# Optimization experiments

Measured on AMD Instinct MI355X. Metric: run time of the kernel, lower is better.

Reference implementation:

```python
import jax, jax.numpy as jnp
import numpy as np

# ---- static config (from xib add_argument defaults / chosen production sizes) ----
B, L = 16, 50            # batch, text length
LU, KU, DIM = 60, 100, 60
V, MAXVL = 2000, 10      # vocab size, max vocab word length (J)
MIN_WL, MAX_WL = 4, 10   # min/max extracted word length
NE = MAX_WL - MIN_WL + 1 # number of len_e candidates
INS_DEL_COST = 3.5       # min_ins_del_cost
UNEXTRACTED_PROB = 0.01
CONTEXT_WEIGHT = 0.1     # weight for context (conv) log-probs
NEG = -9999.9


def setup_inputs() -> dict:
    key = jax.random.key(0)
    ks = jax.random.split(key, 8)
    unit_id_seqs = jax.random.randint(ks[0], (B, L), 0, LU)
    lengths = 10 + jax.random.randint(ks[1], (B,), 0, L - 9)  # in [10, L]
    unit_repr = jax.random.normal(ks[2], (KU, DIM), jnp.float32)
    aligner_weight = 0.1 * jax.random.normal(ks[3], (LU, KU), jnp.float32)
    conv_w = jax.random.normal(ks[4], (DIM, DIM, 3), jnp.float32) / np.sqrt(3.0 * DIM)
    conv_b = jnp.zeros((DIM,), jnp.float32)
    vocab_ids = jax.random.randint(ks[5], (V, MAXVL), 0, KU)
    vocab_lengths = MIN_WL + jax.random.randint(ks[6], (V,), 0, MAXVL - MIN_WL + 1)
    return dict(unit_id_seqs=unit_id_seqs, lengths=lengths, unit_repr=unit_repr,
                aligner_weight=aligner_weight, conv_w=conv_w, conv_b=conv_b,
                vocab_ids=vocab_ids, vocab_lengths=vocab_lengths)


def reference(unit_id_seqs, lengths, unit_repr, aligner_weight, conv_w, conv_b,
              vocab_ids, vocab_lengths):
    # ---- G2P layer: embedding-as-matmul + Conv1d over length ----
    ku_char_repr = aligner_weight @ unit_repr                 # (LU, DIM)
    emb = ku_char_repr[unit_id_seqs]                          # (B, L, DIM)
    x = jnp.swapaxes(emb, 1, 2)                               # (B, DIM, L)
    y = jax.lax.conv_general_dilated(x, conv_w, (1,), 'SAME',
                                     dimension_numbers=('NCH', 'OIH', 'NCH'))
    word_repr = jnp.swapaxes(y + conv_b[None, :, None], 1, 2)  # (B, L, DIM)
    char_log_probs = jax.nn.log_softmax(ku_char_repr @ unit_repr.T, axis=-1)  # (LU, KU)
    alignment = jnp.exp(char_log_probs)
    ctx_log_probs = jax.nn.log_softmax(word_repr @ unit_repr.T, axis=-1)      # (B, L, KU)
    # per-position substitution log prob against each known unit
    pos_lp = char_log_probs[unit_id_seqs] + CONTEXT_WEIGHT * ctx_log_probs    # (B, L, KU)
    sub = pos_lp[:, :, vocab_ids]                                             # (B, L, V, J)
    sub = jnp.pad(sub, ((0, 0), (0, MAX_WL), (0, 0), (0, 0)), constant_values=NEG)
    J = MAXVL
    # ---- edit-distance style DP over (span char i, vocab char j), vectorized
    # over (batch, start position, vocab). prev[b,s,j,v] = f[i-1][j].
    j_ar = jnp.arange(J + 1, dtype=sub.dtype)
    prev = jnp.broadcast_to((-INS_DEL_COST * j_ar)[None, None, :, None], (B, L, J + 1, V))
    vl_idx = jnp.broadcast_to(vocab_lengths[None, None, None, :].astype(jnp.int32), (B, L, 1, V))
    lls = []
    for i in range(1, MAX_WL + 1):          # fixed small loop (<=10)
        sub_i = sub[:, i - 1:i - 1 + L]     # (B, L, V, J): char at position s+i-1
        row = [jnp.full((B, L, V), -INS_DEL_COST * i, dtype=sub.dtype)]
        for j in range(1, J + 1):           # fixed small loop (<=10)
            diag = prev[:, :, j - 1, :] + sub_i[:, :, :, j - 1]
            up = prev[:, :, j, :] - INS_DEL_COST
            left = row[j - 1] - INS_DEL_COST
            row.append(jnp.maximum(diag, jnp.maximum(up, left)))
        prev = jnp.stack(row, axis=2)       # (B, L, J+1, V)
        if i >= MIN_WL:                     # matched ll for word length i
            lls.append(jnp.take_along_axis(prev, vl_idx, axis=2)[:, :, 0, :])
    ll = jnp.stack(lls, axis=2)             # (B, L, NE, V) = matches.ll
    # ---- viability mask + unextracted penalty, pick best candidate ----
    starts = jnp.arange(L)
    word_lens = MIN_WL + jnp.arange(NE)
    viable = (starts[None, :, None] + word_lens[None, None, :]) <= lengths[:, None, None]  # (B,L,NE)
    unextracted = (lengths[:, None, None] - word_lens[None, None, :]).astype(ll.dtype)     # (B,1,NE)
    score = (ll + jnp.where(viable, 0.0, NEG)[..., None]
             + (unextracted * np.log(UNEXTRACTED_PROB))[..., None, :, None][:, 0])
    flat = score.reshape(B, L * NE * V)
    best_idx = jnp.argmax(flat, axis=1)
    best_matched_ll = jnp.max(flat, axis=1)
    start = best_idx // (NE * V)
    e_idx = (best_idx // V) % NE
    best_matched_vocab = best_idx % V
    end = start + MIN_WL + e_idx - 1
    return start, end, best_matched_ll, best_matched_vocab, alignment
```

## Files before the change

kernel.cpp:

```cpp
#include <hip/hip_runtime.h>
#include <math.h>
#include <stdint.h>

#define B_ 16
#define L_ 50
#define LU_ 60
#define KU_ 100
#define DIM_ 60
#define V_ 2000
#define MAXVL_ 10
#define MIN_WL_ 4
#define MAX_WL_ 10
#define NE_ 7
#define IDC_ 3.5f
#define LOG_UNEXT_ (-4.6051701859880913680359829093687f)
#define CTXW_ 0.1f

#define WS_PLP  0
#define WS_BEST_BYTES (80000u * 4u)
#define BEST_STRIDE 8

#define URP_ 61
#define CWP_ 61
#define TSP_ 12

__global__ __launch_bounds__(256) void ctx_kernel(
    const int* __restrict__ uid,
    const float* __restrict__ unit_repr,
    const float* __restrict__ aligner_w,
    const float* __restrict__ conv_w,
    const float* __restrict__ conv_b,
    float* __restrict__ ws_plp,
    float* __restrict__ out_align,
    unsigned long long* __restrict__ g_best)
{
  int bl = blockIdx.x;
  int b = bl / L_, l = bl % L_;
  int t = threadIdx.x;
  __shared__ float s_ur[KU_ * URP_];
  __shared__ float s_cw[3 * DIM_ * CWP_];
  __shared__ float s_aw[3 * KU_];
  __shared__ float sx[3 * DIM_];
  __shared__ float s_kur[DIM_];
  __shared__ float swr[DIM_];
  __shared__ float sclp[KU_];
  __shared__ float slog[KU_];
  __shared__ float salg[KU_];
  __shared__ float sls[3];

  if (bl == 0 && t < B_) g_best[t * BEST_STRIDE] = 0ull;

  const float4* ur4 = (const float4*)unit_repr;
  for (int k = t; k < (KU_ * DIM_) / 4; k += 256) {
    float4 v = ur4[k];
    int i0 = 4 * k;
    s_ur[((i0 + 0) / DIM_) * URP_ + ((i0 + 0) % DIM_)] = v.x;
    s_ur[((i0 + 1) / DIM_) * URP_ + ((i0 + 1) % DIM_)] = v.y;
    s_ur[((i0 + 2) / DIM_) * URP_ + ((i0 + 2) % DIM_)] = v.z;
    s_ur[((i0 + 3) / DIM_) * URP_ + ((i0 + 3) % DIM_)] = v.w;
  }
  const float4* cw4 = (const float4*)conv_w;
  for (int k = t; k < (DIM_ * DIM_ * 3) / 4; k += 256) {
    float4 v = cw4[k];
    int i0 = 4 * k;
    float vv[4] = {v.x, v.y, v.z, v.w};
#pragma unroll
    for (int e = 0; e < 4; ++e) {
      int idx = i0 + e;
      int o = idx / (3 * DIM_), id = idx % (3 * DIM_);
      s_cw[id * CWP_ + o] = vv[e];
    }
  }
  int ud[3];
#pragma unroll
  for (int d = 0; d < 3; ++d) {
    int ld = l + d - 1;
    ud[d] = (ld >= 0 && ld < L_) ? uid[b * L_ + ld] : -1;
  }
  for (int i = t; i < 3 * KU_; i += 256) {
    int d = i / KU_, k = i - d * KU_;
    s_aw[i] = (ud[d] >= 0) ? aligner_w[ud[d] * KU_ + k] : 0.f;
  }
  __syncthreads();

  if (t < 3 * DIM_) {
    int d = t / DIM_, c = t - d * DIM_;
    float acc = 0.f;
    for (int k = 0; k < KU_; ++k) acc += s_aw[d * KU_ + k] * s_ur[k * URP_ + c];
    sx[t] = acc;
  } else if (bl < LU_ && t >= 192 && t < 192 + DIM_) {
    int c = t - 192;
    float acc = 0.f;
    for (int k = 0; k < KU_; ++k) acc += aligner_w[bl * KU_ + k] * s_ur[k * URP_ + c];
    s_kur[c] = acc;
  }
  __syncthreads();

  if (t < DIM_) {
    float acc = conv_b[t];
    for (int i = 0; i < DIM_; ++i) {
      acc += sx[0 * DIM_ + i] * s_cw[(i * 3 + 0) * CWP_ + t];
      acc += sx[1 * DIM_ + i] * s_cw[(i * 3 + 1) * CWP_ + t];
      acc += sx[2 * DIM_ + i] * s_cw[(i * 3 + 2) * CWP_ + t];
    }
    swr[t] = acc;
  } else if (t >= 64 && t < 64 + KU_) {
    int j = t - 64;
    float acc = 0.f;
    for (int d = 0; d < DIM_; ++d) acc += sx[DIM_ + d] * s_ur[j * URP_ + d];
    sclp[j] = acc;
  }
  __syncthreads();

  if (t < KU_) {
    float acc = 0.f;
    for (int d = 0; d < DIM_; ++d) acc += swr[d] * s_ur[t * URP_ + d];
    slog[t] = acc;
  } else if (bl < LU_ && t >= 128 && t < 128 + KU_) {
    int j = t - 128;
    float acc = 0.f;
    for (int d = 0; d < DIM_; ++d) acc += s_kur[d] * s_ur[j * URP_ + d];
    salg[j] = acc;
  }
  __syncthreads();

  {
    int w = t >> 6, lane = t & 63;
    int nred = (bl < LU_) ? 3 : 2;
    if (w < nred) {
      const float* arr = (w == 0) ? sclp : (w == 1) ? slog : salg;
      float v1 = arr[lane];
      float v2 = (lane < KU_ - 64) ? arr[64 + lane] : -1e30f;
      float mx = fmaxf(v1, v2);
#pragma unroll
      for (int off = 32; off > 0; off >>= 1)
        mx = fmaxf(mx, __shfl_xor(mx, off));
      float s = expf(v1 - mx) + ((lane < KU_ - 64) ? expf(v2 - mx) : 0.f);
#pragma unroll
      for (int off = 32; off > 0; off >>= 1)
        s += __shfl_xor(s, off);
      if (lane == 0) sls[w] = mx + logf(s);
    }
  }
  __syncthreads();

  if (t < KU_) {
    float pos = (sclp[t] - sls[0]) + CTXW_ * (slog[t] - sls[1]);
    ws_plp[bl * KU_ + t] = pos;
    if (bl < LU_) out_align[bl * KU_ + t] = expf(salg[t] - sls[2]);
  }
}

__global__ __launch_bounds__(256) void dp_kernel(
    const int* __restrict__ lengths,
    const int* __restrict__ vocab_ids,
    const int* __restrict__ vocab_lengths,
    const float* __restrict__ ws_plp,
    unsigned long long* __restrict__ g_best)
{
  int bl = blockIdx.x;
  int b = bl / L_, l = bl % L_;
  int len_b = lengths[b];
  int imax = len_b - l;
  if (imax > MAX_WL_) imax = MAX_WL_;
  if (imax < MIN_WL_) return;

  __shared__ float sT[KU_ * TSP_];
  __shared__ unsigned long long swave[4];
  int t = threadIdx.x;
  {
    int n = imax * KU_;
    for (int idx = t; idx < n; idx += 256) {
      int i = idx / KU_, k = idx - i * KU_;
      sT[k * TSP_ + i] = ws_plp[(bl + i) * KU_ + k];
    }
  }
  __syncthreads();

  int v0 = blockIdx.y * 512 + t;
  int v1 = v0 + 256;
  bool has1 = (v1 < V_);
  int vid0[MAXVL_], vid1[MAXVL_];
#pragma unroll
  for (int j = 0; j < MAXVL_; ++j) vid0[j] = vocab_ids[v0 * MAXVL_ + j];
  if (has1) {
#pragma unroll
    for (int j = 0; j < MAXVL_; ++j) vid1[j] = vocab_ids[v1 * MAXVL_ + j];
  } else {
#pragma unroll
    for (int j = 0; j < MAXVL_; ++j) vid1[j] = 0;
  }
  int vlen0 = vocab_lengths[v0];
  int vlen1 = has1 ? vocab_lengths[v1] : MIN_WL_;
  bool tail = (imax > 8);

  float A0[MAXVL_ + 1], A1[MAXVL_ + 1];
  float sv0[NE_], sv1[NE_];
#pragma unroll
  for (int e = 0; e < NE_; ++e) { sv0[e] = 0.f; sv1[e] = 0.f; }
#pragma unroll
  for (int i = 0; i <= MAXVL_; ++i) {
    A0[i] = -IDC_ * (float)i;
    A1[i] = A0[i];
  }

#pragma unroll
  for (int j = 1; j <= MAXVL_; ++j) {
    const float* c0 = &sT[vid0[j - 1] * TSP_];
    const float* c1 = &sT[vid1[j - 1] * TSP_];
    float4 a0 = *(const float4*)(c0);
    float4 m0 = *(const float4*)(c0 + 4);
    float4 a1 = *(const float4*)(c1);
    float4 m1 = *(const float4*)(c1 + 4);
    float2 e0 = make_float2(0.f, 0.f), e1 = make_float2(0.f, 0.f);
    if (tail) {
      e0 = *(const float2*)(c0 + 8);
      e1 = *(const float2*)(c1 + 8);
    }
    float s0[MAXVL_] = {a0.x, a0.y, a0.z, a0.w, m0.x, m0.y, m0.z, m0.w, e0.x, e0.y};
    float s1[MAXVL_] = {a1.x, a1.y, a1.z, a1.w, m1.x, m1.y, m1.z, m1.w, e1.x, e1.y};
    float B0[MAXVL_ + 1], B1[MAXVL_ + 1];
    B0[0] = -IDC_ * (float)j;
    B1[0] = B0[0];
#pragma unroll
    for (int i = 1; i <= MAXVL_; ++i) {
      B0[i] = fmaxf(A0[i - 1] + s0[i - 1], fmaxf(A0[i], B0[i - 1]) - IDC_);
      B1[i] = fmaxf(A1[i - 1] + s1[i - 1], fmaxf(A1[i], B1[i - 1]) - IDC_);
    }
    if (j == vlen0) {
#pragma unroll
      for (int e = 0; e < NE_; ++e) sv0[e] = B0[MIN_WL_ + e];
    }
    if (j == vlen1) {
#pragma unroll
      for (int e = 0; e < NE_; ++e) sv1[e] = B1[MIN_WL_ + e];
    }
#pragma unroll
    for (int i = 0; i <= MAXVL_; ++i) { A0[i] = B0[i]; A1[i] = B1[i]; }
  }

  unsigned long long bestKey = 0ull;
#pragma unroll
  for (int e = 0; e < NE_; ++e) {
    int i = MIN_WL_ + e;
    if (i <= imax) {
      float unext = (float)(len_b - i) * LOG_UNEXT_;
      unsigned int idx_base = (unsigned int)(l * (NE_ * V_) + e * V_);
      {
        float score = sv0[e] + unext;
        unsigned int u = __float_as_uint(score);
        u = (u & 0x80000000u) ? ~u : (u | 0x80000000u);
        unsigned long long key =
            ((unsigned long long)u << 32) |
            (unsigned long long)(~(idx_base + (unsigned int)v0));
        if (key > bestKey) bestKey = key;
      }
      if (has1) {
        float score = sv1[e] + unext;
        unsigned int u = __float_as_uint(score);
        u = (u & 0x80000000u) ? ~u : (u | 0x80000000u);
        unsigned long long key =
            ((unsigned long long)u << 32) |
            (unsigned long long)(~(idx_base + (unsigned int)v1));
        if (key > bestKey) bestKey = key;
      }
    }
  }

#pragma unroll
  for (int off = 32; off > 0; off >>= 1) {
    unsigned long long o = __shfl_down(bestKey, off);
    if (o > bestKey) bestKey = o;
  }
  int wid = t >> 6;
  if ((t & 63) == 0) swave[wid] = bestKey;
  __syncthreads();
  if (t == 0) {
    unsigned long long k0 = swave[0];
    for (int w = 1; w < 4; ++w)
      if (swave[w] > k0) k0 = swave[w];
    atomicMax(g_best + (size_t)b * BEST_STRIDE, k0);
  }
}

__global__ void decode_kernel(const unsigned long long* __restrict__ g_best,
                              float* __restrict__ out)
{
  int t = threadIdx.x;
  if (t < B_) {
    unsigned long long key = g_best[t * BEST_STRIDE];
    unsigned int u = (unsigned int)(key >> 32);
    unsigned int idx = ~((unsigned int)(key & 0xFFFFFFFFull));
    unsigned int bits = (u & 0x80000000u) ? (u & 0x7FFFFFFFu) : ~u;
    float val = __uint_as_float(bits);
    int start = (int)(idx / (NE_ * V_));
    int rem = (int)(idx % (NE_ * V_));
    int e = rem / V_;
    int vv = rem % V_;
    out[t] = (float)start;
    out[B_ + t] = (float)(start + MIN_WL_ + e - 1);
    out[2 * B_ + t] = val;
    out[3 * B_ + t] = (float)vv;
  }
}

extern "C" void kernel_launch(void* const* d_in, const int* in_sizes, int n_in,
                              void* d_out, int out_size, void* d_ws, size_t ws_size,
                              hipStream_t stream)
{
  const int* uid            = (const int*)d_in[0];
  const int* lengths        = (const int*)d_in[1];
  const float* unit_repr    = (const float*)d_in[2];
  const float* aligner_w    = (const float*)d_in[3];
  const float* conv_w       = (const float*)d_in[4];
  const float* conv_b       = (const float*)d_in[5];
  const int* vocab_ids      = (const int*)d_in[6];
  const int* vocab_lengths  = (const int*)d_in[7];
  float* out = (float*)d_out;
  float* ws_f = (float*)d_ws;
  unsigned long long* g_best =
      (unsigned long long*)((char*)d_ws + WS_BEST_BYTES);

  ctx_kernel<<<B_ * L_, 256, 0, stream>>>(uid, unit_repr, aligner_w, conv_w,
                                          conv_b, ws_f + WS_PLP, out + 4 * B_,
                                          g_best);
  dim3 g3(B_ * L_, 4);
  dp_kernel<<<g3, 256, 0, stream>>>(lengths, vocab_ids, vocab_lengths,
                                    ws_f + WS_PLP, g_best);
  decode_kernel<<<1, 64, 0, stream>>>(g_best, out);
}
```

Before: 118.1 us.

## Batch four text positions per ctx block and pack vocab ids in DP

The context kernel now handles four consecutive text positions per block (13 blocks per batch row instead of 50), so the unit_repr and conv weight staging into shared memory is amortised over more work and the embeddings of neighbouring positions are shared. The DP kernel packs the 10 vocab ids into three 32-bit registers as bytes to cut register pressure. It also folds the best-key computation into the DP loop at the matching word length, dropping the saved-value arrays. The tail-load guard is removed, so the DP always reads 10 columns from shared memory. Fewer ctx blocks means less parallelism in that stage.

```diff
diff --git a/kernel.cpp b/kernel.cpp
--- a/kernel.cpp
+++ b/kernel.cpp
@@ -15,6 +15,7 @@
 #define IDC_ 3.5f
 #define LOG_UNEXT_ (-4.6051701859880913680359829093687f)
 #define CTXW_ 0.1f
+#define NQ_ 13
 
 #define WS_PLP  0
 #define WS_BEST_BYTES (80000u * 4u)
@@ -34,21 +35,24 @@
     float* __restrict__ out_align,
     unsigned long long* __restrict__ g_best)
 {
-  int bl = blockIdx.x;
-  int b = bl / L_, l = bl % L_;
+  int blk = blockIdx.x;
+  int b = blk / NQ_, q = blk % NQ_;
+  int l0 = 4 * q;
+  int npos = (l0 + 4 <= L_) ? 4 : (L_ - l0);
+  int alr = (blk < LU_) ? blk : -1;
   int t = threadIdx.x;
+
   __shared__ float s_ur[KU_ * URP_];
   __shared__ float s_cw[3 * DIM_ * CWP_];
-  __shared__ float s_aw[3 * KU_];
-  __shared__ float sx[3 * DIM_];
-  __shared__ float s_kur[DIM_];
-  __shared__ float swr[DIM_];
-  __shared__ float sclp[KU_];
-  __shared__ float slog[KU_];
+  __shared__ float s_aw[7 * KU_];
+  __shared__ float s_kx[7 * DIM_];
+  __shared__ float swr[4 * DIM_];
+  __shared__ float sclp[4 * KU_];
+  __shared__ float sctx[4 * KU_];
   __shared__ float salg[KU_];
-  __shared__ float sls[3];
-
-  if (bl == 0 && t < B_) g_best[t * BEST_STRIDE] = 0ull;
+  __shared__ float sls[9];
+
+  if (blk == 0 && t < B_) g_best[t * BEST_STRIDE] = 0ull;
 
   const float4* ur4 = (const float4*)unit_repr;
   for (int k = t; k < (KU_ * DIM_) / 4; k += 256) {
@@ -71,84 +75,101 @@
       s_cw[id * CWP_ + o] = vv[e];
     }
   }
-  int ud[3];
-#pragma unroll
-  for (int d = 0; d < 3; ++d) {
-    int ld = l + d - 1;
-    ud[d] = (ld >= 0 && ld < L_) ? uid[b * L_ + ld] : -1;
-  }
-  for (int i = t; i < 3 * KU_; i += 256) {
-    int d = i / KU_, k = i - d * KU_;
-    s_aw[i] = (ud[d] >= 0) ? aligner_w[ud[d] * KU_ + k] : 0.f;
-  }
-  __syncthreads();
-
-  if (t < 3 * DIM_) {
-    int d = t / DIM_, c = t - d * DIM_;
+  for (int i = t; i < 7 * KU_; i += 256) {
+    int m = i / KU_, k = i - m * KU_;
+    float w = 0.f;
+    if (m < 6) {
+      int ld = l0 - 1 + m;
+      if (ld >= 0 && ld < L_) {
+        int u = uid[b * L_ + ld];
+        w = aligner_w[u * KU_ + k];
+      }
+    } else if (alr >= 0) {
+      w = aligner_w[alr * KU_ + k];
+    }
+    s_aw[i] = w;
+  }
+  __syncthreads();
+
+  for (int idx = t; idx < 7 * DIM_; idx += 256) {
+    int m = idx / DIM_, c = idx - m * DIM_;
     float acc = 0.f;
-    for (int k = 0; k < KU_; ++k) acc += s_aw[d * KU_ + k] * s_ur[k * URP_ + c];
-    sx[t] = acc;
-  } else if (bl < LU_ && t >= 192 && t < 192 + DIM_) {
-    int c = t - 192;
-    float acc = 0.f;
-    for (int k = 0; k < KU_; ++k) acc += aligner_w[bl * KU_ + k] * s_ur[k * URP_ + c];
-    s_kur[c] = acc;
-  }
-  __syncthreads();
-
-  if (t < DIM_) {
-    float acc = conv_b[t];
-    for (int i = 0; i < DIM_; ++i) {
-      acc += sx[0 * DIM_ + i] * s_cw[(i * 3 + 0) * CWP_ + t];
-      acc += sx[1 * DIM_ + i] * s_cw[(i * 3 + 1) * CWP_ + t];
-      acc += sx[2 * DIM_ + i] * s_cw[(i * 3 + 2) * CWP_ + t];
-    }
-    swr[t] = acc;
-  } else if (t >= 64 && t < 64 + KU_) {
-    int j = t - 64;
-    float acc = 0.f;
-    for (int d = 0; d < DIM_; ++d) acc += sx[DIM_ + d] * s_ur[j * URP_ + d];
-    sclp[j] = acc;
-  }
-  __syncthreads();
-
-  if (t < KU_) {
-    float acc = 0.f;
-    for (int d = 0; d < DIM_; ++d) acc += swr[d] * s_ur[t * URP_ + d];
-    slog[t] = acc;
-  } else if (bl < LU_ && t >= 128 && t < 128 + KU_) {
-    int j = t - 128;
-    float acc = 0.f;
-    for (int d = 0; d < DIM_; ++d) acc += s_kur[d] * s_ur[j * URP_ + d];
-    salg[j] = acc;
+    for (int k = 0; k < KU_; ++k) acc += s_aw[m * KU_ + k] * s_ur[k * URP_ + c];
+    s_kx[idx] = acc;
+  }
+  __syncthreads();
+
+  for (int idx = t; idx < 240 + 4 * KU_; idx += 256) {
+    if (idx < 240) {
+      int p = idx / DIM_, o = idx - p * DIM_;
+      float acc = conv_b[o];
+      for (int i = 0; i < DIM_; ++i) {
+        acc += s_kx[(p + 0) * DIM_ + i] * s_cw[(i * 3 + 0) * CWP_ + o];
+        acc += s_kx[(p + 1) * DIM_ + i] * s_cw[(i * 3 + 1) * CWP_ + o];
+        acc += s_kx[(p + 2) * DIM_ + i] * s_cw[(i * 3 + 2) * CWP_ + o];
+      }
+      swr[p * DIM_ + o] = acc;
+    } else {
+      int r = idx - 240;
+      int p = r / KU_, j = r - p * KU_;
+      float acc = 0.f;
+      for (int d = 0; d < DIM_; ++d) acc += s_kx[(p + 1) * DIM_ + d] * s_ur[j * URP_ + d];
+      sclp[r] = acc;
+    }
+  }
+  __syncthreads();
+
+  for (int idx = t; idx < 4 * KU_ + KU_; idx += 256) {
+    if (idx < 4 * KU_) {
+      int p = idx / KU_, j = idx - p * KU_;
+      float acc = 0.f;
+      for (int d = 0; d < DIM_; ++d) acc += swr[p * DIM_ + d] * s_ur[j * URP_ + d];
+      sctx[idx] = acc;
+    } else {
+      int j = idx - 4 * KU_;
+      float acc = 0.f;
+      for (int d = 0; d < DIM_; ++d) acc += s_kx[6 * DIM_ + d] * s_ur[j * URP_ + d];
+      salg[j] = acc;
+    }
   }
   __syncthreads();
 
   {
-    int w = t >> 6, lane = t & 63;
-    int nred = (bl < LU_) ? 3 : 2;
-    if (w < nred) {
-      const float* arr = (w == 0) ? sclp : (w == 1) ? slog : salg;
-      float v1 = arr[lane];
-      float v2 = (lane < KU_ - 64) ? arr[64 + lane] : -1e30f;
-      float mx = fmaxf(v1, v2);
-#pragma unroll
-      for (int off = 32; off > 0; off >>= 1)
-        mx = fmaxf(mx, __shfl_xor(mx, off));
-      float s = expf(v1 - mx) + ((lane < KU_ - 64) ? expf(v2 - mx) : 0.f);
-#pragma unroll
-      for (int off = 32; off > 0; off >>= 1)
-        s += __shfl_xor(s, off);
-      if (lane == 0) sls[w] = mx + logf(s);
-    }
-  }
-  __syncthreads();
-
-  if (t < KU_) {
-    float pos = (sclp[t] - sls[0]) + CTXW_ * (slog[t] - sls[1]);
-    ws_plp[bl * KU_ + t] = pos;
-    if (bl < LU_) out_align[bl * KU_ + t] = expf(salg[t] - sls[2]);
-  }
+    int g = t >> 5, lane = t & 31;
+#pragma unroll
+    for (int round = 0; round < 2; ++round) {
+      int r = round * 8 + g;
+      if (r < 9) {
+        const float* arr = (r == 8) ? salg
+                          : ((r & 1) ? &sctx[(r >> 1) * KU_] : &sclp[(r >> 1) * KU_]);
+        float v1 = arr[lane];
+        float v2 = arr[32 + lane];
+        float v3 = arr[64 + lane];
+        float v4 = (lane < KU_ - 96) ? arr[96 + lane] : -1e30f;
+        float mx = fmaxf(fmaxf(v1, v2), fmaxf(v3, v4));
+#pragma unroll
+        for (int off = 16; off > 0; off >>= 1)
+          mx = fmaxf(mx, __shfl_xor(mx, off));
+        float s = expf(v1 - mx) + expf(v2 - mx) + expf(v3 - mx) +
+                  ((lane < KU_ - 96) ? expf(v4 - mx) : 0.f);
+#pragma unroll
+        for (int off = 16; off > 0; off >>= 1)
+          s += __shfl_xor(s, off);
+        if (lane == 0) sls[r] = mx + logf(s);
+      }
+    }
+  }
+  __syncthreads();
+
+  for (int idx = t; idx < 4 * KU_; idx += 256) {
+    int p = idx / KU_, j = idx - p * KU_;
+    if (p < npos) {
+      float pos = (sclp[idx] - sls[2 * p]) + CTXW_ * (sctx[idx] - sls[2 * p + 1]);
+      ws_plp[(b * L_ + l0 + p) * KU_ + j] = pos;
+    }
+  }
+  if (alr >= 0 && t < KU_)
+    out_align[alr * KU_ + t] = expf(salg[t] - sls[8]);
 }
 
 __global__ __launch_bounds__(256) void dp_kernel(
@@ -180,43 +201,38 @@
   int v0 = blockIdx.y * 512 + t;
   int v1 = v0 + 256;
   bool has1 = (v1 < V_);
-  int vid0[MAXVL_], vid1[MAXVL_];
-#pragma unroll
-  for (int j = 0; j < MAXVL_; ++j) vid0[j] = vocab_ids[v0 * MAXVL_ + j];
+  unsigned p0[3] = {0u, 0u, 0u}, p1[3] = {0u, 0u, 0u};
+#pragma unroll
+  for (int j = 0; j < MAXVL_; ++j)
+    p0[j >> 2] |= ((unsigned)vocab_ids[v0 * MAXVL_ + j]) << ((j & 3) * 8);
   if (has1) {
 #pragma unroll
-    for (int j = 0; j < MAXVL_; ++j) vid1[j] = vocab_ids[v1 * MAXVL_ + j];
-  } else {
-#pragma unroll
-    for (int j = 0; j < MAXVL_; ++j) vid1[j] = 0;
+    for (int j = 0; j < MAXVL_; ++j)
+      p1[j >> 2] |= ((unsigned)vocab_ids[v1 * MAXVL_ + j]) << ((j & 3) * 8);
   }
   int vlen0 = vocab_lengths[v0];
-  int vlen1 = has1 ? vocab_lengths[v1] : MIN_WL_;
-  bool tail = (imax > 8);
+  int vlen1 = has1 ? vocab_lengths[v1] : 0;
 
   float A0[MAXVL_ + 1], A1[MAXVL_ + 1];
-  float sv0[NE_], sv1[NE_];
-#pragma unroll
-  for (int e = 0; e < NE_; ++e) { sv0[e] = 0.f; sv1[e] = 0.f; }
 #pragma unroll
   for (int i = 0; i <= MAXVL_; ++i) {
     A0[i] = -IDC_ * (float)i;
     A1[i] = A0[i];
   }
+  unsigned long long bestKey = 0ull;
 
 #pragma unroll
   for (int j = 1; j <= MAXVL_; ++j) {
-    const float* c0 = &sT[vid0[j - 1] * TSP_];
-    const float* c1 = &sT[vid1[j - 1] * TSP_];
+    int k0 = (int)((p0[(j - 1) >> 2] >> (((j - 1) & 3) * 8)) & 0xFFu);
+    int k1 = (int)((p1[(j - 1) >> 2] >> (((j - 1) & 3) * 8)) & 0xFFu);
+    const float* c0 = &sT[k0 * TSP_];
+    const float* c1 = &sT[k1 * TSP_];
     float4 a0 = *(const float4*)(c0);
     float4 m0 = *(const float4*)(c0 + 4);
+    float2 e0 = *(const float2*)(c0 + 8);
     float4 a1 = *(const float4*)(c1);
     float4 m1 = *(const float4*)(c1 + 4);
-    float2 e0 = make_float2(0.f, 0.f), e1 = make_float2(0.f, 0.f);
-    if (tail) {
-      e0 = *(const float2*)(c0 + 8);
-      e1 = *(const float2*)(c1 + 8);
-    }
+    float2 e1 = *(const float2*)(c1 + 8);
     float s0[MAXVL_] = {a0.x, a0.y, a0.z, a0.w, m0.x, m0.y, m0.z, m0.w, e0.x, e0.y};
     float s1[MAXVL_] = {a1.x, a1.y, a1.z, a1.w, m1.x, m1.y, m1.z, m1.w, e1.x, e1.y};
     float B0[MAXVL_ + 1], B1[MAXVL_ + 1];
@@ -229,42 +245,36 @@
     }
     if (j == vlen0) {
 #pragma unroll
-      for (int e = 0; e < NE_; ++e) sv0[e] = B0[MIN_WL_ + e];
+      for (int e = 0; e < NE_; ++e) {
+        int i = MIN_WL_ + e;
+        if (i <= imax) {
+          float score = B0[i] + (float)(len_b - i) * LOG_UNEXT_;
+          unsigned int idx = (unsigned int)(l * (NE_ * V_) + e * V_ + v0);
+          unsigned int u = __float_as_uint(score);
+          u = (u & 0x80000000u) ? ~u : (u | 0x80000000u);
+          unsigned long long key =
+              ((unsigned long long)u << 32) | (unsigned long long)(~idx);
+          if (key > bestKey) bestKey = key;
+        }
+      }
     }
     if (j == vlen1) {
 #pragma unroll
-      for (int e = 0; e < NE_; ++e) sv1[e] = B1[MIN_WL_ + e];
+      for (int e = 0; e < NE_; ++e) {
+        int i = MIN_WL_ + e;
+        if (i <= imax) {
+          float score = B1[i] + (float)(len_b - i) * LOG_UNEXT_;
+          unsigned int idx = (unsigned int)(l * (NE_ * V_) + e * V_ + v1);
+          unsigned int u = __float_as_uint(score);
+          u = (u & 0x80000000u) ? ~u : (u | 0x80000000u);
+          unsigned long long key =
+              ((unsigned long long)u << 32) | (unsigned long long)(~idx);
+          if (key > bestKey) bestKey = key;
+        }
+      }
     }
 #pragma unroll
     for (int i = 0; i <= MAXVL_; ++i) { A0[i] = B0[i]; A1[i] = B1[i]; }
-  }
-
-  unsigned long long bestKey = 0ull;
-#pragma unroll
-  for (int e = 0; e < NE_; ++e) {
-    int i = MIN_WL_ + e;
-    if (i <= imax) {
-      float unext = (float)(len_b - i) * LOG_UNEXT_;
-      unsigned int idx_base = (unsigned int)(l * (NE_ * V_) + e * V_);
-      {
-        float score = sv0[e] + unext;
-        unsigned int u = __float_as_uint(score);
-        u = (u & 0x80000000u) ? ~u : (u | 0x80000000u);
-        unsigned long long key =
-            ((unsigned long long)u << 32) |
-            (unsigned long long)(~(idx_base + (unsigned int)v0));
-        if (key > bestKey) bestKey = key;
-      }
-      if (has1) {
-        float score = sv1[e] + unext;
-        unsigned int u = __float_as_uint(score);
-        u = (u & 0x80000000u) ? ~u : (u | 0x80000000u);
-        unsigned long long key =
-            ((unsigned long long)u << 32) |
-            (unsigned long long)(~(idx_base + (unsigned int)v1));
-        if (key > bestKey) bestKey = key;
-      }
-    }
   }
 
 #pragma unroll
@@ -321,9 +331,9 @@
   unsigned long long* g_best =
       (unsigned long long*)((char*)d_ws + WS_BEST_BYTES);
 
-  ctx_kernel<<<B_ * L_, 256, 0, stream>>>(uid, unit_repr, aligner_w, conv_w,
-                                          conv_b, ws_f + WS_PLP, out + 4 * B_,
-                                          g_best);
+  ctx_kernel<<<B_ * NQ_, 256, 0, stream>>>(uid, unit_repr, aligner_w, conv_w,
+                                           conv_b, ws_f + WS_PLP, out + 4 * B_,
+                                           g_best);
   dim3 g3(B_ * L_, 4);
   dp_kernel<<<g3, 256, 0, stream>>>(lengths, vocab_ids, vocab_lengths,
                                     ws_f + WS_PLP, g_best);
```

Result: faster. 113.0 us (-4.4%).
